# Kernel optimization log

Measured on AMD Instinct MI355X. Metric: run time of the kernel, lower is better.

## Reference

```python
import jax, jax.numpy as jnp
import numpy as np

N, C_IN, H, W = 16, 32, 512, 512
C_OUT, K, STRIDE = 32, 3, 1


def setup_inputs() -> dict:
    key = jax.random.key(0)
    k1, k2, k3 = jax.random.split(key, 3)
    x = jax.random.normal(k1, (N, C_IN, H, W), dtype=jnp.float32)
    weight = jax.random.normal(k2, (C_OUT, C_IN, K, K), dtype=jnp.float32) * 0.05
    bias = jax.random.normal(k3, (C_OUT,), dtype=jnp.float32) * 0.05
    return {"x": x, "weight": weight, "bias": bias}


def reference(x, weight, bias):
    # Direct 2D convolution, NCHW / OIHW, stride 1, no padding (VALID),
    # matching the module's per-pixel multiply+sum with padding=0.
    out = jax.lax.conv_general_dilated(
        x, weight,
        window_strides=(STRIDE, STRIDE),
        padding="VALID",
        dimension_numbers=("NCHW", "OIHW", "NCHW"),
    )
    return out + bias[None, :, None, None]
```

## Files before the change

### kernel.cpp

```cpp
#include <hip/hip_runtime.h>


namespace {
constexpr int NI    = 16;
constexpr int C_IN  = 32;
constexpr int HI    = 512;
constexpr int WI    = 512;
constexpr int C_OUT = 32;
constexpr int HO    = 510;
constexpr int WO    = 510;

constexpr int RT    = 6;
constexpr int PT    = 64;
constexpr int XROWS = RT + 2;
constexpr int XCOLS = PT + 2;
constexpr int PSTR  = 36;
constexpr int HIWI  = HI * WI;
}

typedef __attribute__((ext_vector_type(4))) float  floatx4;
typedef __attribute__((ext_vector_type(8))) __bf16 bf16x8;
typedef __attribute__((ext_vector_type(4))) __bf16 bf16x4;
typedef __attribute__((ext_vector_type(4))) unsigned short ushortx4;

__global__ void conv_wprep(const float* __restrict__ w, __bf16* __restrict__ ws) {
  const int t = threadIdx.x;
  for (int i = t; i < 9 * 2 * 64 * 8; i += 256) {
    const int j    = i & 7;
    const int lane = (i >> 3) & 63;
    const int h    = (i >> 9) & 1;
    const int tap  = i >> 10;
    const int co   = h * 16 + (lane & 15);
    const int ci   = (lane >> 4) * 8 + j;
    ws[i] = (__bf16)w[(co * C_IN + ci) * 9 + tap];
  }
}

__global__ __launch_bounds__(256, 4)
void conv3x3_mfma(const float* __restrict__ x, const __bf16* __restrict__ ws,
                  const float* __restrict__ bias, float* __restrict__ out) {
  __shared__ unsigned short lds[XROWS * XCOLS * PSTR];

  const int t    = threadIdx.x;
  const int lane = t & 63;
  const int wv   = t >> 6;
  const int quad = lane >> 4;
  const int l16  = lane & 15;

  const int x0 = blockIdx.x * PT;
  const int y0 = blockIdx.y * RT;
  const int n  = blockIdx.z;

  for (int p = t; p < XROWS * XCOLS; p += 256) {
    const int row = p / XCOLS;
    const int col = p - row * XCOLS;
    int gx = x0 + col;
    if (gx > WI - 1) gx = WI - 1;
    const float* xp = x + ((size_t)(n * C_IN) * HI + (y0 + row)) * WI + gx;
    union { __bf16 b[32]; ushortx4 q[8]; } pk;
#pragma unroll
    for (int ci = 0; ci < C_IN; ++ci)
      pk.b[ci] = (__bf16)xp[ci * HIWI];
    unsigned short* dst = &lds[p * PSTR];
#pragma unroll
    for (int k = 0; k < 8; ++k)
      *reinterpret_cast<ushortx4*>(dst + k * 4) = pk.q[k];
  }

  bf16x8 afrag[9][2];
#pragma unroll
  for (int tap = 0; tap < 9; ++tap)
#pragma unroll
    for (int h = 0; h < 2; ++h)
      afrag[tap][h] = *reinterpret_cast<const bf16x8*>(ws + ((tap * 2 + h) * 64 + lane) * 8);

  float b0[4], b1[4];
#pragma unroll
  for (int r = 0; r < 4; ++r) {
    b0[r] = bias[quad * 4 + r];
    b1[r] = bias[quad * 4 + r + 16];
  }

  __syncthreads();

  const int pbase  = wv * 16 + l16;
  const int px     = x0 + pbase;
  const bool valid = px < WO;

  for (int row = 0; row < RT; ++row) {
    floatx4 acc0 = {b0[0], b0[1], b0[2], b0[3]};
    floatx4 acc1 = {b1[0], b1[1], b1[2], b1[3]};
#pragma unroll
    for (int ky = 0; ky < 3; ++ky)
#pragma unroll
      for (int kx = 0; kx < 3; ++kx) {
        union { bf16x8 v; bf16x4 h[2]; } bf;
        const int base = ((row + ky) * XCOLS + pbase + kx) * PSTR + quad * 8;
        bf.h[0] = *reinterpret_cast<const bf16x4*>(&lds[base]);
        bf.h[1] = *reinterpret_cast<const bf16x4*>(&lds[base + 4]);
        acc0 = __builtin_amdgcn_mfma_f32_16x16x32_bf16(afrag[ky * 3 + kx][0], bf.v, acc0, 0, 0, 0);
        acc1 = __builtin_amdgcn_mfma_f32_16x16x32_bf16(afrag[ky * 3 + kx][1], bf.v, acc1, 0, 0, 0);
      }
    if (valid) {
      float* op = out + ((size_t)(n * C_OUT + quad * 4) * HO + (y0 + row)) * WO + px;
#pragma unroll
      for (int r = 0; r < 4; ++r) {
        op[r * (HO * WO)]        = acc0[r];
        op[(16 + r) * (HO * WO)] = acc1[r];
      }
    }
  }
}

extern "C" void kernel_launch(void* const* d_in, const int* in_sizes, int n_in,
                              void* d_out, int out_size, void* d_ws, size_t ws_size,
                              hipStream_t stream) {
  const float* x    = (const float*)d_in[0];
  const float* w    = (const float*)d_in[1];
  const float* bias = (const float*)d_in[2];
  float* out        = (float*)d_out;
  __bf16* ws        = (__bf16*)d_ws;

  conv_wprep<<<dim3(1), 256, 0, stream>>>(w, ws);

  dim3 grid(WI / PT, HO / RT, NI);
  conv3x3_mfma<<<grid, 256, 0, stream>>>(x, ws, bias, out);
}
```

Before: 1.001 ms.

## Give each wave a private ring of input rows and prefetch the next row during MFMA

Each wave now stages only its own 18-pixel-wide column strip into a private 4-slot LDS ring buffer, so the block-wide __syncthreads disappears. Global loads for row r+3 are issued before the MFMAs for row r and written to LDS afterwards, overlapping memory latency with compute. The cost is duplicated halo loads between neighbouring waves, more registers (launch bounds lowered to 3 blocks per SM), and it relies on each wave only reading LDS it wrote itself, with no barrier. It also writes scalar bf16 values to LDS instead of vectorised stores.

After: 1.008 ms. Within noise of the previous version (+0.7%).

```diff
diff --git a/kernel.cpp b/kernel.cpp
--- a/kernel.cpp
+++ b/kernel.cpp
@@ -12,16 +12,17 @@
 
 constexpr int RT    = 6;
 constexpr int PT    = 64;
-constexpr int XROWS = RT + 2;
-constexpr int XCOLS = PT + 2;
+constexpr int WPX   = 18;
+constexpr int SLOTS = 4;
 constexpr int PSTR  = 36;
+constexpr int SLOTW = WPX * PSTR;
+constexpr int WREG  = SLOTS * SLOTW;
 constexpr int HIWI  = HI * WI;
 }
 
 typedef __attribute__((ext_vector_type(4))) float  floatx4;
 typedef __attribute__((ext_vector_type(8))) __bf16 bf16x8;
 typedef __attribute__((ext_vector_type(4))) __bf16 bf16x4;
-typedef __attribute__((ext_vector_type(4))) unsigned short ushortx4;
 
 __global__ void conv_wprep(const float* __restrict__ w, __bf16* __restrict__ ws) {
   const int t = threadIdx.x;
@@ -36,10 +37,10 @@
   }
 }
 
-__global__ __launch_bounds__(256, 4)
+__global__ __launch_bounds__(256, 3)
 void conv3x3_mfma(const float* __restrict__ x, const __bf16* __restrict__ ws,
                   const float* __restrict__ bias, float* __restrict__ out) {
-  __shared__ unsigned short lds[XROWS * XCOLS * PSTR];
+  __shared__ __bf16 lds[4 * WREG];
 
   const int t    = threadIdx.x;
   const int lane = t & 63;
@@ -51,21 +52,33 @@
   const int y0 = blockIdx.y * RT;
   const int n  = blockIdx.z;
 
-  for (int p = t; p < XROWS * XCOLS; p += 256) {
-    const int row = p / XCOLS;
-    const int col = p - row * XCOLS;
-    int gx = x0 + col;
+  const float* xn = x + (size_t)n * C_IN * HIWI;
+
+  int A[9], L[9];
+#pragma unroll
+  for (int j = 0; j < 9; ++j) {
+    const int u  = j * 64 + lane;
+    const int px = u % WPX;
+    const int ci = u / WPX;
+    int gx = x0 + wv * 16 + px;
     if (gx > WI - 1) gx = WI - 1;
-    const float* xp = x + ((size_t)(n * C_IN) * HI + (y0 + row)) * WI + gx;
-    union { __bf16 b[32]; ushortx4 q[8]; } pk;
+    A[j] = ci * HIWI + gx;
+    L[j] = wv * WREG + px * PSTR + ci;
+  }
+
+  auto issue = [&](int gr, float (&st)[9]) {
+    const float* rbase = xn + (size_t)(y0 + gr) * WI;
 #pragma unroll
-    for (int ci = 0; ci < C_IN; ++ci)
-      pk.b[ci] = (__bf16)xp[ci * HIWI];
-    unsigned short* dst = &lds[p * PSTR];
+    for (int j = 0; j < 9; ++j) st[j] = rbase[A[j]];
+  };
+  auto commit = [&](int gr, float (&st)[9]) {
+    const int so = (gr & (SLOTS - 1)) * SLOTW;
 #pragma unroll
-    for (int k = 0; k < 8; ++k)
-      *reinterpret_cast<ushortx4*>(dst + k * 4) = pk.q[k];
-  }
+    for (int j = 0; j < 9; ++j) lds[L[j] + so] = (__bf16)st[j];
+  };
+
+  float s0[9], s1[9], s2[9];
+  issue(0, s0); issue(1, s1); issue(2, s2);
 
   bf16x8 afrag[9][2];
 #pragma unroll
@@ -81,26 +94,33 @@
     b1[r] = bias[quad * 4 + r + 16];
   }
 
-  __syncthreads();
+  commit(0, s0); commit(1, s1); commit(2, s2);
 
-  const int pbase  = wv * 16 + l16;
-  const int px     = x0 + pbase;
+  const int px     = x0 + wv * 16 + l16;
   const bool valid = px < WO;
+  const int ldsw   = wv * WREG + l16 * PSTR + quad * 8;
 
+  float st[9];
+#pragma unroll
   for (int row = 0; row < RT; ++row) {
+    if (row < RT - 1) issue(row + 3, st);
+
     floatx4 acc0 = {b0[0], b0[1], b0[2], b0[3]};
     floatx4 acc1 = {b1[0], b1[1], b1[2], b1[3]};
 #pragma unroll
     for (int ky = 0; ky < 3; ++ky)
 #pragma unroll
       for (int kx = 0; kx < 3; ++kx) {
+        const int base = ldsw + ((row + ky) & (SLOTS - 1)) * SLOTW + kx * PSTR;
         union { bf16x8 v; bf16x4 h[2]; } bf;
-        const int base = ((row + ky) * XCOLS + pbase + kx) * PSTR + quad * 8;
         bf.h[0] = *reinterpret_cast<const bf16x4*>(&lds[base]);
         bf.h[1] = *reinterpret_cast<const bf16x4*>(&lds[base + 4]);
         acc0 = __builtin_amdgcn_mfma_f32_16x16x32_bf16(afrag[ky * 3 + kx][0], bf.v, acc0, 0, 0, 0);
         acc1 = __builtin_amdgcn_mfma_f32_16x16x32_bf16(afrag[ky * 3 + kx][1], bf.v, acc1, 0, 0, 0);
       }
+
+    if (row < RT - 1) commit(row + 3, st);
+
     if (valid) {
       float* op = out + ((size_t)(n * C_OUT + quad * 4) * HO + (y0 + row)) * WO + px;
 #pragma unroll
```
